# Kernel tuning notes

Hardware: AMD Instinct MI355X
Metric: run time of the kernel (lower is better)

Reference implementation:

```python
import jax, jax.numpy as jnp
import numpy as np
from itertools import combinations

ADD = 3  # max subset size (init arg `add`)


def setup_inputs() -> dict:
    key = jax.random.key(0)
    k1, _ = jax.random.split(key)
    # fuzzy membership values in [0, 1]
    x = jax.random.uniform(k1, (131072, 16), dtype=jnp.float32)
    lambda_ = jnp.asarray(0.3, dtype=jnp.float32)  # learnable scalar parameter
    return {"x": x, "lambda_": lambda_}


def reference(x, lambda_):
    """Dubois t-norm over all column subsets of size 2..ADD.

    Vectorized per subset size k: gather all C(n, k) subsets at once
    ([B, Ck, k]) and fold the binary Dubois t-norm
        T(a, b) = a*b / max(max(a, b), lambda)
    over the k axis, instead of looping per combination.
    """
    n = x.shape[1]
    outs = [x]  # order matches original: identity columns first, then k=2, k=3, ...
    for k in range(2, ADD + 1):
        idx = np.array(list(combinations(range(n), k)), dtype=np.int32)  # [Ck, k]
        subset = x[:, idx]  # [B, Ck, k]
        hidden = subset[:, :, 0]
        for i in range(1, k):  # fold over subset elements (left-to-right, as original)
            s = subset[:, :, i]
            hidden = hidden * s / jnp.maximum(jnp.maximum(hidden, s), lambda_)
        outs.append(hidden)
    return jnp.concatenate(outs, axis=1)  # [B, n + sum_k C(n,k)] = [B, 696]
```

## Files before the change

### kernel.cpp

```cpp
#include <hip/hip_runtime.h>

#define NCOLS 16
#define NPAIR 120
#define NTRIP 560
#define OUTC  (NCOLS + NPAIR + NTRIP)
#define NREG  11

struct ColTab { unsigned int c[NREG * 64]; };

constexpr ColTab make_cols() {
    ColTab t{};
    int q = 0;
    for (int i = 0; i < NCOLS; ++i)
        t.c[q++] = (unsigned)i | ((unsigned)i << 8) | ((unsigned)i << 16) | (0u << 24);
    for (int i = 0; i < NCOLS; ++i)
        for (int j = i + 1; j < NCOLS; ++j)
            t.c[q++] = (unsigned)i | ((unsigned)j << 8) | ((unsigned)j << 16) | (1u << 24);
    for (int i = 0; i < NCOLS; ++i)
        for (int j = i + 1; j < NCOLS; ++j)
            for (int k = j + 1; k < NCOLS; ++k)
                t.c[q++] = (unsigned)i | ((unsigned)j << 8) | ((unsigned)k << 16) | (2u << 24);
    while (q < NREG * 64) t.c[q++] = 0u;
    return t;
}

__device__ const ColTab d_cols = make_cols();

__device__ __forceinline__ float tnorm(float a, float b, float lam) {
    float m = fmaxf(fmaxf(a, b), lam);
    return a * b * __builtin_amdgcn_rcpf(m);
}

__global__ __launch_bounds__(256) void dubois_kernel(
    const float* __restrict__ x, const float* __restrict__ lam_p,
    float* __restrict__ out, int B, int iters, int nwaves)
{
    const int lane  = threadIdx.x & 63;
    const int gwave = (blockIdx.x * blockDim.x + threadIdx.x) >> 6;
    const float lam = lam_p[0];

    unsigned int tab[NREG];
    #pragma unroll
    for (int r = 0; r < NREG; ++r)
        tab[r] = d_cols.c[lane + r * 64];

    for (int it = 0; it < iters; ++it) {
        const int row = gwave + it * nwaves;
        if (row >= B) break;

        float v = x[(size_t)row * NCOLS + (lane & 15)];
        float* __restrict__ orow = out + (size_t)row * OUTC;

        float res[NREG];
        #pragma unroll
        for (int r = 0; r < NREG; ++r) {
            unsigned int e = tab[r];
            float a  = __shfl(v, (int)(e & 255u));
            float b  = __shfl(v, (int)((e >> 8) & 255u));
            float c  = __shfl(v, (int)((e >> 16) & 255u));
            float t1 = tnorm(a, b, lam);
            float t2 = tnorm(t1, c, lam);
            unsigned int op = e >> 24;
            res[r] = (op == 0u) ? a : ((op == 1u) ? t1 : t2);
        }

        #pragma unroll
        for (int r = 0; r < NREG; ++r) {
            int c = lane + r * 64;
            if (r < NREG - 1 || c < OUTC)
                orow[c] = res[r];
        }
    }
}

extern "C" void kernel_launch(void* const* d_in, const int* in_sizes, int n_in,
                              void* d_out, int out_size, void* d_ws, size_t ws_size,
                              hipStream_t stream) {
    const float* x   = (const float*)d_in[0];
    const float* lam = (const float*)d_in[1];
    float* out = (float*)d_out;

    const int B = in_sizes[0] / NCOLS;
    const int threads = 256;
    const int blocks  = 2048;
    const int nwaves  = blocks * (threads / 64);
    const int iters   = (B + nwaves - 1) / nwaves;

    dubois_kernel<<<blocks, threads, 0, stream>>>(x, lam, out, B, iters, nwaves);
}
```

Before: 397.8 us.

## Process four rows per wave with 16-byte nontemporal vector stores

Each wave now handles four rows at once: 16 lanes per row, and each lane computes four consecutive output columns and writes them with one 16-byte nontemporal store. The column table is packed as uint4 entries read from the constant table inside the loop, and the input load covers 64 contiguous floats. This targets a store-bound kernel by using wider, fully coalesced writes and fewer loop iterations per row. In exchange each lane does four times the shuffles per iteration and re-reads the table each iteration. B is assumed divisible by 4.

```diff
diff --git a/kernel.cpp b/kernel.cpp
--- a/kernel.cpp
+++ b/kernel.cpp
@@ -4,23 +4,33 @@
 #define NPAIR 120
 #define NTRIP 560
 #define OUTC  (NCOLS + NPAIR + NTRIP)
-#define NREG  11
+#define NQUAD 174
+#define QITER 11
 
-struct ColTab { unsigned int c[NREG * 64]; };
+typedef float  vfloat4 __attribute__((ext_vector_type(4)));
+typedef unsigned int vuint4 __attribute__((ext_vector_type(4)));
+
+struct ColTab { vuint4 q[QITER * 16]; };
 
 constexpr ColTab make_cols() {
     ColTab t{};
-    int q = 0;
+    unsigned tmp[QITER * 16 * 4] = {};
+    int qn = 0;
     for (int i = 0; i < NCOLS; ++i)
-        t.c[q++] = (unsigned)i | ((unsigned)i << 8) | ((unsigned)i << 16) | (0u << 24);
+        tmp[qn++] = (unsigned)i;
     for (int i = 0; i < NCOLS; ++i)
         for (int j = i + 1; j < NCOLS; ++j)
-            t.c[q++] = (unsigned)i | ((unsigned)j << 8) | ((unsigned)j << 16) | (1u << 24);
+            tmp[qn++] = (unsigned)i | ((unsigned)j << 8) | (1u << 24);
     for (int i = 0; i < NCOLS; ++i)
         for (int j = i + 1; j < NCOLS; ++j)
             for (int k = j + 1; k < NCOLS; ++k)
-                t.c[q++] = (unsigned)i | ((unsigned)j << 8) | ((unsigned)k << 16) | (2u << 24);
-    while (q < NREG * 64) t.c[q++] = 0u;
+                tmp[qn++] = (unsigned)i | ((unsigned)j << 8) | ((unsigned)k << 16) | (2u << 24);
+    for (int f = 0; f < QITER * 16; ++f) {
+        t.q[f][0] = tmp[4 * f + 0];
+        t.q[f][1] = tmp[4 * f + 1];
+        t.q[f][2] = tmp[4 * f + 2];
+        t.q[f][3] = tmp[4 * f + 3];
+    }
     return t;
 }
 
@@ -31,44 +41,46 @@
     return a * b * __builtin_amdgcn_rcpf(m);
 }
 
+__device__ __forceinline__ float colval(unsigned e, float v, int gbase, float lam) {
+    float a = __shfl(v, gbase + (int)(e & 15u));
+    float b = __shfl(v, gbase + (int)((e >> 8) & 15u));
+    float c = __shfl(v, gbase + (int)((e >> 16) & 15u));
+    float t1 = tnorm(a, b, lam);
+    float t2 = tnorm(t1, c, lam);
+    unsigned op = e >> 24;
+    return (op == 0u) ? a : ((op == 1u) ? t1 : t2);
+}
+
 __global__ __launch_bounds__(256) void dubois_kernel(
     const float* __restrict__ x, const float* __restrict__ lam_p,
-    float* __restrict__ out, int B, int iters, int nwaves)
+    float* __restrict__ out, int ngroups, int iters, int nwaves)
 {
     const int lane  = threadIdx.x & 63;
+    const int sub   = lane & 15;
+    const int gbase = lane & 48;
     const int gwave = (blockIdx.x * blockDim.x + threadIdx.x) >> 6;
     const float lam = lam_p[0];
 
-    unsigned int tab[NREG];
-    #pragma unroll
-    for (int r = 0; r < NREG; ++r)
-        tab[r] = d_cols.c[lane + r * 64];
+    for (int it = 0; it < iters; ++it) {
+        const int grp = gwave + it * nwaves;
+        if (grp >= ngroups) break;
 
-    for (int it = 0; it < iters; ++it) {
-        const int row = gwave + it * nwaves;
-        if (row >= B) break;
+        float v = x[(size_t)grp * 64 + lane];
 
-        float v = x[(size_t)row * NCOLS + (lane & 15)];
-        float* __restrict__ orow = out + (size_t)row * OUTC;
-
-        float res[NREG];
-        #pragma unroll
-        for (int r = 0; r < NREG; ++r) {
-            unsigned int e = tab[r];
-            float a  = __shfl(v, (int)(e & 255u));
-            float b  = __shfl(v, (int)((e >> 8) & 255u));
-            float c  = __shfl(v, (int)((e >> 16) & 255u));
-            float t1 = tnorm(a, b, lam);
-            float t2 = tnorm(t1, c, lam);
-            unsigned int op = e >> 24;
-            res[r] = (op == 0u) ? a : ((op == 1u) ? t1 : t2);
-        }
+        const int myrow = grp * 4 + (lane >> 4);
+        vfloat4* __restrict__ orow4 = reinterpret_cast<vfloat4*>(out + (size_t)myrow * OUTC);
 
         #pragma unroll
-        for (int r = 0; r < NREG; ++r) {
-            int c = lane + r * 64;
-            if (r < NREG - 1 || c < OUTC)
-                orow[c] = res[r];
+        for (int r = 0; r < QITER; ++r) {
+            const int f = r * 16 + sub;
+            const vuint4 e = d_cols.q[f];
+            vfloat4 o;
+            o[0] = colval(e[0], v, gbase, lam);
+            o[1] = colval(e[1], v, gbase, lam);
+            o[2] = colval(e[2], v, gbase, lam);
+            o[3] = colval(e[3], v, gbase, lam);
+            if (r < QITER - 1 || f < NQUAD)
+                __builtin_nontemporal_store(o, orow4 + f);
         }
     }
 }
@@ -81,10 +93,11 @@
     float* out = (float*)d_out;
 
     const int B = in_sizes[0] / NCOLS;
+    const int ngroups = B / 4;
     const int threads = 256;
     const int blocks  = 2048;
     const int nwaves  = blocks * (threads / 64);
-    const int iters   = (B + nwaves - 1) / nwaves;
+    const int iters   = (ngroups + nwaves - 1) / nwaves;
 
-    dubois_kernel<<<blocks, threads, 0, stream>>>(x, lam, out, B, iters, nwaves);
+    dubois_kernel<<<blocks, threads, 0, stream>>>(x, lam, out, ngroups, iters, nwaves);
 }
```

Result: slower. 431.7 us (+8.5%).

## Compute one row per thread with float4 stores and reuse pair t-norms

Applied to the files above, without the earlier changes.

Replaces the wave-per-row mapping, which used shuffles and a lookup table, with one thread per row. Each thread loads its 16 inputs as four float4 vectors, computes each pair t-norm once and reuses it for all triples that share that pair, and writes 16-byte vector stores. This removes the shuffles and the redundant pair recomputation. The cost is that stores across a wave are strided by the 2784-byte row pitch and no longer coalesced, which may hurt a kernel that is bound by write bandwidth.

```diff
diff --git a/kernel.cpp b/kernel.cpp
--- a/kernel.cpp
+++ b/kernel.cpp
@@ -3,28 +3,11 @@
 #define NCOLS 16
 #define NPAIR 120
 #define NTRIP 560
-#define OUTC  (NCOLS + NPAIR + NTRIP)
-#define NREG  11
+#define OUTC  696
+#define PQ0   4
+#define TQ0   34
 
-struct ColTab { unsigned int c[NREG * 64]; };
-
-constexpr ColTab make_cols() {
-    ColTab t{};
-    int q = 0;
-    for (int i = 0; i < NCOLS; ++i)
-        t.c[q++] = (unsigned)i | ((unsigned)i << 8) | ((unsigned)i << 16) | (0u << 24);
-    for (int i = 0; i < NCOLS; ++i)
-        for (int j = i + 1; j < NCOLS; ++j)
-            t.c[q++] = (unsigned)i | ((unsigned)j << 8) | ((unsigned)j << 16) | (1u << 24);
-    for (int i = 0; i < NCOLS; ++i)
-        for (int j = i + 1; j < NCOLS; ++j)
-            for (int k = j + 1; k < NCOLS; ++k)
-                t.c[q++] = (unsigned)i | ((unsigned)j << 8) | ((unsigned)k << 16) | (2u << 24);
-    while (q < NREG * 64) t.c[q++] = 0u;
-    return t;
-}
-
-__device__ const ColTab d_cols = make_cols();
+typedef float v4f __attribute__((ext_vector_type(4)));
 
 __device__ __forceinline__ float tnorm(float a, float b, float lam) {
     float m = fmaxf(fmaxf(a, b), lam);
@@ -33,42 +16,55 @@
 
 __global__ __launch_bounds__(256) void dubois_kernel(
     const float* __restrict__ x, const float* __restrict__ lam_p,
-    float* __restrict__ out, int B, int iters, int nwaves)
+    float* __restrict__ out, int B)
 {
-    const int lane  = threadIdx.x & 63;
-    const int gwave = (blockIdx.x * blockDim.x + threadIdx.x) >> 6;
+    const int row = blockIdx.x * 256 + threadIdx.x;
+    if (row >= B) return;
     const float lam = lam_p[0];
 
-    unsigned int tab[NREG];
+    const v4f* __restrict__ xr = reinterpret_cast<const v4f*>(x + (size_t)row * NCOLS);
+    v4f xq0 = xr[0], xq1 = xr[1], xq2 = xr[2], xq3 = xr[3];
+
+    float xv[NCOLS];
     #pragma unroll
-    for (int r = 0; r < NREG; ++r)
-        tab[r] = d_cols.c[lane + r * 64];
+    for (int c = 0; c < 4; ++c) {
+        xv[c]      = xq0[c];
+        xv[4 + c]  = xq1[c];
+        xv[8 + c]  = xq2[c];
+        xv[12 + c] = xq3[c];
+    }
 
-    for (int it = 0; it < iters; ++it) {
-        const int row = gwave + it * nwaves;
-        if (row >= B) break;
+    v4f* __restrict__ o4 = reinterpret_cast<v4f*>(out + (size_t)row * OUTC);
 
-        float v = x[(size_t)row * NCOLS + (lane & 15)];
-        float* __restrict__ orow = out + (size_t)row * OUTC;
+    o4[0] = xq0; o4[1] = xq1; o4[2] = xq2; o4[3] = xq3;
 
-        float res[NREG];
+    float sp[4];
+    float st[4];
+    int cp = 0;
+    int ct = 0;
+
+    #pragma unroll
+    for (int i = 0; i < NCOLS; ++i) {
         #pragma unroll
-        for (int r = 0; r < NREG; ++r) {
-            unsigned int e = tab[r];
-            float a  = __shfl(v, (int)(e & 255u));
-            float b  = __shfl(v, (int)((e >> 8) & 255u));
-            float c  = __shfl(v, (int)((e >> 16) & 255u));
-            float t1 = tnorm(a, b, lam);
-            float t2 = tnorm(t1, c, lam);
-            unsigned int op = e >> 24;
-            res[r] = (op == 0u) ? a : ((op == 1u) ? t1 : t2);
-        }
+        for (int j = i + 1; j < NCOLS; ++j) {
+            const float pv = tnorm(xv[i], xv[j], lam);
 
-        #pragma unroll
-        for (int r = 0; r < NREG; ++r) {
-            int c = lane + r * 64;
-            if (r < NREG - 1 || c < OUTC)
-                orow[c] = res[r];
+            sp[cp & 3] = pv;
+            if ((cp & 3) == 3) {
+                v4f t; t[0] = sp[0]; t[1] = sp[1]; t[2] = sp[2]; t[3] = sp[3];
+                o4[PQ0 + (cp >> 2)] = t;
+            }
+            ++cp;
+
+            #pragma unroll
+            for (int k = j + 1; k < NCOLS; ++k) {
+                st[ct & 3] = tnorm(pv, xv[k], lam);
+                if ((ct & 3) == 3) {
+                    v4f t; t[0] = st[0]; t[1] = st[1]; t[2] = st[2]; t[3] = st[3];
+                    o4[TQ0 + (ct >> 2)] = t;
+                }
+                ++ct;
+            }
         }
     }
 }
@@ -82,9 +78,6 @@
 
     const int B = in_sizes[0] / NCOLS;
     const int threads = 256;
-    const int blocks  = 2048;
-    const int nwaves  = blocks * (threads / 64);
-    const int iters   = (B + nwaves - 1) / nwaves;
-
-    dubois_kernel<<<blocks, threads, 0, stream>>>(x, lam, out, B, iters, nwaves);
+    const int blocks  = (B + threads - 1) / threads;
+    dubois_kernel<<<blocks, threads, 0, stream>>>(x, lam, out, B);
 }
```

Result: slower. 517.5 us (+30.1%).
